# Kernel optimization log

Measured on AMD Instinct MI355X. Metric: run time of the kernel, lower is better.

The kernel has to match this reference:

```python
import jax, jax.numpy as jnp
import numpy as np
from jax.scipy.special import logsumexp

B, T, D = 16, 512, 768
S, H, O = 4, 48, 48
EMISS_W = 0.5  # args.emiss_nn_weight


def setup_inputs() -> dict:
    key = jax.random.key(0)
    ks = jax.random.split(key, 6)
    emb = jax.random.normal(ks[0], (B, T, D), jnp.float32)
    # obs must be valid per-source distributions over n_obs (log is taken)
    obs = jax.nn.softmax(2.0 * jax.random.normal(ks[1], (B, T, S, O), jnp.float32), axis=-1)
    # default prior init: priors = 0.001, priors[0] = 1, param = log(priors)
    p = jnp.full((H,), 0.001, jnp.float32).at[0].set(1.0)
    state_priors = jnp.log(p)
    unnorm_trans = jax.random.normal(ks[2], (H, H), jnp.float32)
    unnorm_emiss = jnp.zeros((S, H, O), jnp.float32)
    # xavier_uniform with relu gain for the per-source emission Linears
    bound = np.sqrt(2.0) * np.sqrt(6.0 / (D + H * O))
    W_emiss = jax.random.uniform(ks[3], (S, H * O, D), jnp.float32, -bound, bound)
    b_emiss = jnp.zeros((S, H * O), jnp.float32)
    seq_lengths = jax.random.randint(ks[4], (B,), T // 2, T + 1).astype(jnp.int32)
    seq_lengths = seq_lengths.at[0].set(T)  # max length == T
    return dict(emb=emb, obs=obs, state_priors=state_priors, unnorm_trans=unnorm_trans,
                unnorm_emiss=unnorm_emiss, W_emiss=W_emiss, b_emiss=b_emiss,
                seq_lengths=seq_lengths)


def _lognorm(x):
    return x - logsumexp(x, axis=-1, keepdims=True)


def reference(emb, obs, state_priors, unnorm_trans, unnorm_emiss, W_emiss, b_emiss, seq_lengths):
    lp = jax.nn.log_softmax(state_priors)                 # [H]
    log_trans = jax.nn.log_softmax(unnorm_trans, axis=-1)  # [H,H] (constant over b,t)
    emiss = jax.nn.softmax(unnorm_emiss, axis=-1)          # [S,H,O]

    # neural emissions: per-source Linear(d_emb -> H*O), softmax over O
    logits = jnp.einsum('btd,sod->btso', emb, W_emiss) + b_emiss  # [B,T,S,H*O]
    nn_emiss = jax.nn.softmax(logits.reshape(B, T, S, H, O), axis=-1)
    # (nn_trans is computed by NeuralModule in the original but discarded)

    log_emiss = jnp.log((1.0 - EMISS_W) * emiss[None, None] + EMISS_W * nn_emiss)  # [B,T,S,H,O]
    # log_matmul over obs axis, then sum over sources -> [B,T,H]
    lep = logsumexp(log_emiss + jnp.log(obs)[:, :, :, None, :], axis=-1).sum(axis=2)

    # forward recursion (normalized each step)
    a0 = _lognorm(lp + lep[:, 0])                          # [B,H]

    def fstep(a_prev, lep_t):
        a = _lognorm(lep_t + logsumexp(a_prev[:, :, None] + log_trans[None], axis=1))
        return a, a

    _, alphas = jax.lax.scan(fstep, a0, jnp.swapaxes(lep[:, 1:], 0, 1))
    log_alpha = jnp.concatenate([a0[:, None], jnp.swapaxes(alphas, 0, 1)], axis=1)  # [B,T,H]

    # backward recursion: beta[t] = logsumexp_j(trans[i,j] + lep[t,j] + beta[t+1,j])
    bT = jnp.zeros((B, H), lep.dtype)

    def bstep(b_next, lep_t):
        b = logsumexp(log_trans[None] + (lep_t + b_next)[:, None, :], axis=2)
        return b, b

    _, betas = jax.lax.scan(bstep, bT, jnp.swapaxes(lep[:, :T - 1], 0, 1), reverse=True)
    log_beta = jnp.concatenate([jnp.swapaxes(betas, 0, 1), bT[:, None]], axis=1)  # [B,T,H]
    # per-example roll by (length - T) along time, as in the original
    log_beta = jax.vmap(lambda b, s: jnp.roll(b, s, axis=0))(log_beta, seq_lengths - T)

    log_gamma = _lognorm(log_alpha + log_beta)             # [B,T,H]

    # xi_t = trans + alpha[t-1] (outer-sum) (lep[t] + beta[t]),  t = 1..T-1
    xi = (log_trans[None, None]
          + log_alpha[:, :-1, :, None]
          + (lep[:, 1:] + log_beta[:, 1:])[:, :, None, :])  # [B,T-1,H,H]
    xi = xi - logsumexp(xi, axis=(-2, -1), keepdims=True)

    log_prior = jnp.mean(jnp.sum(jnp.exp(log_gamma[:, 0]) * lp, axis=-1))

    tran_terms = jnp.sum(jnp.exp(xi) * log_trans[None, None], axis=(-2, -1))  # [B,T-1]
    mask_tr = (jnp.arange(T - 1)[None] < (seq_lengths - 1)[:, None]).astype(lep.dtype)
    log_tran = jnp.mean(jnp.sum(tran_terms * mask_tr, axis=1))

    emis_terms = jnp.sum(jnp.exp(log_gamma) * lep, axis=-1)  # [B,T]
    mask_em = (jnp.arange(T)[None] < seq_lengths[:, None]).astype(lep.dtype)
    log_emis = jnp.mean(jnp.sum(emis_terms * mask_em, axis=1))

    return log_prior + log_tran + log_emis
```

## Files before the change

### kernel.cpp

```cpp
#include <hip/hip_runtime.h>
#include <math.h>

namespace {

constexpr int Bn = 16, Tn = 512, Dn = 768, Sn = 4, Hn = 48, On = 48;
constexpr int Mn = Bn * Tn;
constexpr int Gn = Sn * Hn;
constexpr int Nn = Gn * On;
constexpr float EMISS_W = 0.5f;

constexpr size_t OFF_LP   = 0;
constexpr size_t OFF_LT   = 64;
constexpr size_t OFF_PT   = OFF_LT + Hn*Hn;
constexpr size_t OFF_EM   = OFF_PT + Hn*Hn;
constexpr size_t OFF_LEPP = OFF_EM + (size_t)Sn*Hn*On;
constexpr size_t OFF_LA   = OFF_LEPP + (size_t)Mn*Gn;
constexpr size_t OFF_LB   = OFF_LA + (size_t)Mn*Hn;
constexpr size_t OFF_RED  = OFF_LB + (size_t)Mn*Hn;
constexpr size_t FLOATS_END = OFF_RED + (size_t)Mn;

typedef __attribute__((ext_vector_type(8))) short short8;
typedef __attribute__((ext_vector_type(4))) float f32x4;

__device__ inline float waveSum(float v){
#pragma unroll
  for (int o = 32; o; o >>= 1) v += __shfl_xor(v, o);
  return v;
}

__device__ inline unsigned short f2bf(float f){
  unsigned int u = __float_as_uint(f);
  u += 0x7FFFu + ((u >> 16) & 1u);
  return (unsigned short)(u >> 16);
}

__device__ inline void gload_lds16(const void* g, void* l){
  __builtin_amdgcn_global_load_lds(
      (const __attribute__((address_space(1))) void*)g,
      (__attribute__((address_space(3))) void*)l, 16, 0, 0);
}

__global__ void convprep_kernel(const float* __restrict__ srcA, unsigned short* __restrict__ dstA,
                                int n4a,
                                const float* __restrict__ srcB, unsigned short* __restrict__ dstB,
                                int n4b,
                                const float* __restrict__ sp, const float* __restrict__ ut,
                                const float* __restrict__ ue, float* __restrict__ ws,
                                int nconv){
  const int tid = threadIdx.x;
  if ((int)blockIdx.x == nconv){
    float m = -INFINITY;
    for (int h = 0; h < Hn; ++h) m = fmaxf(m, sp[h]);
    float s = 0.f;
    for (int h = 0; h < Hn; ++h) s += __expf(sp[h] - m);
    float lse = m + __logf(s);
    if (tid < Hn) ws[OFF_LP + tid] = sp[tid] - lse;
    if (tid < Hn){
      const float* row = ut + tid * Hn;
      float mm = -INFINITY;
      for (int j = 0; j < Hn; ++j) mm = fmaxf(mm, row[j]);
      float ss = 0.f;
      for (int j = 0; j < Hn; ++j) ss += __expf(row[j] - mm);
      float l = mm + __logf(ss);
      for (int j = 0; j < Hn; ++j){
        float v = row[j] - l;
        ws[OFF_LT + tid*Hn + j] = v;
        ws[OFF_PT + tid*Hn + j] = __expf(v);
      }
    }
    for (int r = tid; r < Sn*Hn; r += blockDim.x){
      const float* row = ue + (size_t)r * On;
      float mm = -INFINITY;
      for (int o = 0; o < On; ++o) mm = fmaxf(mm, row[o]);
      float ss = 0.f;
      for (int o = 0; o < On; ++o) ss += __expf(row[o] - mm);
      float inv = 1.f/ss;
      for (int o = 0; o < On; ++o) ws[OFF_EM + (size_t)r*On + o] = __expf(row[o]-mm)*inv;
    }
    return;
  }
  int i = blockIdx.x * blockDim.x + tid;
  const float* s2; unsigned short* d; int k;
  if (i < n4a){ s2 = srcA; d = dstA; k = i; }
  else { k = i - n4a; if (k >= n4b) return; s2 = srcB; d = dstB; }
  float4 v = ((const float4*)s2)[k];
  ushort4 r;
  r.x = f2bf(v.x); r.y = f2bf(v.y); r.z = f2bf(v.z); r.w = f2bf(v.w);
  ((ushort4*)d)[k] = r;
}

constexpr int BM = 128, BN = 192, BK = 64;
constexpr int NKT = Dn / BK;

#define GEMM_BAR()  asm volatile("s_barrier" ::: "memory")
#define GEMM_LGKM() asm volatile("s_waitcnt lgkmcnt(0)" ::: "memory")

__global__ __launch_bounds__(256, 2) void gemm_lep_kernel(
    const unsigned short* __restrict__ embB, const unsigned short* __restrict__ WB,
    const float* __restrict__ bm, const float* __restrict__ obs,
    float* __restrict__ ws){
  __shared__ __align__(16) char smem[81920];
  const int tid = threadIdx.x, lane = tid & 63, w = tid >> 6;
  const int bid = blockIdx.y * (Mn/BM) + blockIdx.x;
  const int xcd = bid & 7, j_loc = bid >> 3;
  const int xm = xcd & 3, xn = xcd >> 2;
  const int mloc = j_loc & 15, nloc = j_loc >> 4;
  const int m0 = (xm*16 + mloc) * BM;
  const int by = xn*24 + nloc;
  const int N0 = by * BN;
  const int wm = w & 1, wn = w >> 1;
  const int lm = lane & 15, q = lane >> 4;
  const int key = lm & 7;
  const int srow = lane >> 3, spc = lane & 7;
  const int aoff0 = (q ^ key) << 4;
  const int aoff1 = ((4 + q) ^ key) << 4;

  f32x4 acc[4][6];
#pragma unroll
  for (int i = 0; i < 4; ++i)
#pragma unroll
    for (int j = 0; j < 6; ++j) acc[i][j] = (f32x4){0.f,0.f,0.f,0.f};

  auto stageA = [&](int kt, int i){
    const int idx = w*4 + i;
    const int row = idx*8 + srow;
    const int lc  = spc ^ (row & 7);
    gload_lds16(embB + (size_t)(m0+row)*Dn + kt*BK + lc*8,
                smem + (kt & 1)*16384 + idx*1024);
  };
  auto stageB = [&](int kt, int i){
    const int idx = w*6 + i;
    const int row = idx*8 + srow;
    const int lc  = spc ^ (row & 7);
    gload_lds16(WB + (size_t)(N0+row)*Dn + kt*BK + lc*8,
                smem + 32768 + (kt & 1)*24576 + idx*1024);
  };

#pragma unroll
  for (int i = 0; i < 4; ++i) stageA(0, i);
#pragma unroll
  for (int i = 0; i < 6; ++i) stageB(0, i);
  asm volatile("s_waitcnt vmcnt(0)" ::: "memory");
  GEMM_BAR();

  for (int kt = 0; kt < NKT; ++kt){
    const char* Ab = smem + (kt & 1)*16384;
    const char* Bb = smem + 32768 + (kt & 1)*24576;
    const int pf = kt + 1;
    const bool dopf = pf < NKT;
    short8 af[4], bf[3];

#pragma unroll
    for (int j = 0; j < 3; ++j)
      bf[j] = *(const short8*)(Bb + (wn*96 + j*16 + lm)*128 + aoff0);
#pragma unroll
    for (int i = 0; i < 4; ++i)
      af[i] = *(const short8*)(Ab + (wm*64 + i*16 + lm)*128 + aoff0);
    if (dopf){ stageA(pf,0); stageA(pf,1); stageA(pf,2); stageA(pf,3);
               stageB(pf,0); stageB(pf,1); }
    GEMM_BAR();
    GEMM_LGKM();
    __builtin_amdgcn_s_setprio(1);
#pragma unroll
    for (int i = 0; i < 4; ++i)
#pragma unroll
      for (int j = 0; j < 3; ++j)
        acc[i][j] = __builtin_amdgcn_mfma_f32_16x16x32_bf16(af[i], bf[j], acc[i][j], 0, 0, 0);
    __builtin_amdgcn_s_setprio(0);
    GEMM_BAR();

#pragma unroll
    for (int j = 0; j < 3; ++j)
      bf[j] = *(const short8*)(Bb + (wn*96 + (3+j)*16 + lm)*128 + aoff0);
    if (dopf){ stageB(pf,2); stageB(pf,3); }
    GEMM_BAR();
    GEMM_LGKM();
    __builtin_amdgcn_s_setprio(1);
#pragma unroll
    for (int i = 0; i < 4; ++i)
#pragma unroll
      for (int j = 0; j < 3; ++j)
        acc[i][3+j] = __builtin_amdgcn_mfma_f32_16x16x32_bf16(af[i], bf[j], acc[i][3+j], 0, 0, 0);
    __builtin_amdgcn_s_setprio(0);
    GEMM_BAR();

#pragma unroll
    for (int j = 0; j < 3; ++j)
      bf[j] = *(const short8*)(Bb + (wn*96 + j*16 + lm)*128 + aoff1);
#pragma unroll
    for (int i = 0; i < 4; ++i)
      af[i] = *(const short8*)(Ab + (wm*64 + i*16 + lm)*128 + aoff1);
    if (dopf){ stageB(pf,4); stageB(pf,5); }
    GEMM_BAR();
    GEMM_LGKM();
    __builtin_amdgcn_s_setprio(1);
#pragma unroll
    for (int i = 0; i < 4; ++i)
#pragma unroll
      for (int j = 0; j < 3; ++j)
        acc[i][j] = __builtin_amdgcn_mfma_f32_16x16x32_bf16(af[i], bf[j], acc[i][j], 0, 0, 0);
    __builtin_amdgcn_s_setprio(0);
    GEMM_BAR();

#pragma unroll
    for (int j = 0; j < 3; ++j)
      bf[j] = *(const short8*)(Bb + (wn*96 + (3+j)*16 + lm)*128 + aoff1);
    GEMM_BAR();
    GEMM_LGKM();
    __builtin_amdgcn_s_setprio(1);
#pragma unroll
    for (int i = 0; i < 4; ++i)
#pragma unroll
      for (int j = 0; j < 3; ++j)
        acc[i][3+j] = __builtin_amdgcn_mfma_f32_16x16x32_bf16(af[i], bf[j], acc[i][3+j], 0, 0, 0);
    __builtin_amdgcn_s_setprio(0);
    asm volatile("s_waitcnt vmcnt(0)" ::: "memory");
    GEMM_BAR();
  }

  float* Cp  = (float*)smem;
  float* ext = (float*)(smem + 49408);
  if (tid < 192){
    ext[tid]       = bm[N0 + tid];
    ext[192 + tid] = ws[OFF_EM + N0 + tid];
  }
#pragma unroll
  for (int h = 0; h < 2; ++h){
    if (h) __syncthreads();
    if (wm == h){
#pragma unroll
      for (int i = 0; i < 4; ++i)
#pragma unroll
        for (int j = 0; j < 6; ++j){
          const int col = wn*96 + j*16 + lm;
#pragma unroll
          for (int r = 0; r < 4; ++r){
            const int rowl = i*16 + q*4 + r;
            Cp[rowl*193 + col] = acc[i][j][r];
          }
        }
    }
    __syncthreads();
    {
      const int rowl = tid >> 2, grp = tid & 3;
      const int m = m0 + h*64 + rowl;
      const int g = by*4 + grp;
      const int s2 = g / Hn;
      const float* crow = Cp + rowl*193 + grp*48;
      const float* ob   = obs + ((size_t)m*Sn + s2)*On;
      const float* bi   = ext + grp*48;
      const float* em   = ext + 192 + grp*48;
      float Z = 0.f, pd = 0.f, eo = 0.f;
#pragma unroll
      for (int o = 0; o < On; ++o){
        float e = __expf(crow[o] + bi[o]);
        float obv = ob[o];
        Z += e;
        pd = fmaf(e, obv, pd);
        eo = fmaf(em[o], obv, eo);
      }
      ws[OFF_LEPP + (size_t)m*Gn + g] = __logf((1.f-EMISS_W)*eo + EMISS_W*(pd/Z));
    }
  }
}

constexpr int FBW = 24;
constexpr int FBL = 16;

__global__ __launch_bounds__(64) void fb_kernel(float* __restrict__ ws){
  __shared__ __align__(16) float ldsE[(FBW+FBL)*48];
  __shared__ __align__(16) float ring[2][64];
  const int lane = threadIdx.x;
  const int c    = blockIdx.x;
  const int b    = blockIdx.y;
  const bool fwd = blockIdx.z == 0;
  const bool act = lane < Hn;
  const int t0 = c*FBL, te = t0 + FBL - 1;

  float pt[Hn];
#pragma unroll
  for (int i = 0; i < Hn; ++i)
    pt[i] = act ? (fwd ? ws[OFF_PT + i*Hn + lane] : ws[OFF_PT + lane*Hn + i]) : 0.f;

  int row_lo, nrows, sA, sZ;
  bool exact;
  if (fwd){
    sA = t0 - FBW;
    exact = (sA < 1);
    row_lo = exact ? 0 : sA;
    if (exact) sA = 1;
    sZ = te;
    nrows = te - row_lo + 1;
  } else {
    int th = te + 1 + FBW;
    exact = (th > Tn - 2);
    sA = exact ? Tn - 2 : th - 1;
    sZ = t0;
    row_lo = t0;
    nrows = sA - t0 + 1;
  }

  {
    const float* src = ws + OFF_LEPP + ((size_t)b*Tn + row_lo)*Gn;
    int n4 = nrows * (Hn/4);
    for (int i = lane; i < n4; i += 64){
      int r = i / (Hn/4), h4 = i - r*(Hn/4);
      const float* p = src + (size_t)r*Gn + h4*4;
      float4 a = *(const float4*)(p);
      float4 b2 = *(const float4*)(p + Hn);
      float4 c2 = *(const float4*)(p + 2*Hn);
      float4 d2 = *(const float4*)(p + 3*Hn);
      float4 e;
      e.x = __expf(a.x + b2.x + c2.x + d2.x);
      e.y = __expf(a.y + b2.y + c2.y + d2.y);
      e.z = __expf(a.z + b2.z + c2.z + d2.z);
      e.w = __expf(a.w + b2.w + c2.w + d2.w);
      ((float4*)ldsE)[i] = e;
    }
  }
  __syncthreads();

  if (fwd){
    const size_t laF = OFF_LA + (size_t)b * Tn * Hn;
    float v;
    if (exact){
      v = act ? __expf(ws[OFF_LP + lane]) * ldsE[lane] : 0.f;
      if (c == 0 && act) ws[laF + lane] = v;
    } else {
      v = act ? 1.f : 0.f;
    }
    if (act) ring[0][lane] = v;
    __syncthreads();
    int cur = 0;
    for (int t = sA; t <= sZ; ++t){
      float S = waveSum(v);
      const float* rp = ring[cur];
      float s0=0.f,s1=0.f,s2=0.f,s3=0.f;
#pragma unroll
      for (int i = 0; i < Hn; i += 4){
        float4 a = *(const float4*)(rp + i);
        s0 = fmaf(a.x, pt[i+0], s0); s1 = fmaf(a.y, pt[i+1], s1);
        s2 = fmaf(a.z, pt[i+2], s2); s3 = fmaf(a.w, pt[i+3], s3);
      }
      float sd = (s0+s1)+(s2+s3);
      float e = act ? ldsE[(t - row_lo)*Hn + lane] : 0.f;
      float vn = act ? e * sd * (1.f/S) : 0.f;
      cur ^= 1;
      if (act) ring[cur][lane] = vn;
      __syncthreads();
      if (act && t >= t0) ws[laF + (size_t)t*Hn + lane] = vn;
      v = vn;
    }
  } else {
    const size_t lbF = OFF_LB + (size_t)b * Tn * Hn;
    float v = act ? 1.f : 0.f;
    if (exact && c == (Tn/FBL - 1) && act) ws[lbF + (size_t)(Tn-1)*Hn + lane] = 1.f;
    int cur = 0;
    for (int t = sA; t >= sZ; --t){
      float e = act ? ldsE[(t - row_lo)*Hn + lane] : 0.f;
      float wv = e * v;
      if (act) ring[cur][lane] = wv;
      float S = waveSum(wv);
      __syncthreads();
      const float* rp = ring[cur];
      float s0=0.f,s1=0.f,s2=0.f,s3=0.f;
#pragma unroll
      for (int j = 0; j < Hn; j += 4){
        float4 a = *(const float4*)(rp + j);
        s0 = fmaf(a.x, pt[j+0], s0); s1 = fmaf(a.y, pt[j+1], s1);
        s2 = fmaf(a.z, pt[j+2], s2); s3 = fmaf(a.w, pt[j+3], s3);
      }
      float vn = act ? ((s0+s1)+(s2+s3)) * (1.f/S) : 0.f;
      cur ^= 1;
      if (act && t <= te) ws[lbF + (size_t)t*Hn + lane] = vn;
      v = vn;
    }
  }
}

__global__ __launch_bounds__(256) void gamma_xi_kernel(
    const float* __restrict__ ws_c, float* __restrict__ ws,
    const int* __restrict__ seq_len){
  __shared__ float y_s[Hn], lap_s[Hn];
  __shared__ float red[8];
  const int tid = threadIdx.x;
  const int bid = blockIdx.x;
  const int b = bid >> 9, t = bid & (Tn-1);
  const int len = seq_len[b];
  int tb = t + (Tn - len); if (tb >= Tn) tb -= Tn;
  const size_t bt = (size_t)b*Tn + t;
  float lep = 0.f;
  if (tid < Hn){
    const float* lpp = ws_c + OFF_LEPP + bt*Gn + tid;
    lep = lpp[0] + lpp[Hn] + lpp[2*Hn] + lpp[3*Hn];
    float lb  = ws_c[OFF_LB + ((size_t)b*Tn + tb)*Hn + tid];
    y_s[tid] = __expf(lep) * lb;
    if (t >= 1) lap_s[tid] = ws_c[OFF_LA + (bt-1)*Hn + tid];
  }
  float emis_term = 0.f, prior_term = 0.f;
  if (tid < 64){
    int h = (tid < Hn) ? tid : 0;
    float la  = ws_c[OFF_LA + bt*Hn + h];
    float lb  = ws_c[OFF_LB + ((size_t)b*Tn + tb)*Hn + h];
    float lp  = ws_c[OFF_LP + h];
    float wgt = (tid < Hn) ? la*lb : 0.f;
    float Z = waveSum(wgt);
    float inv = 1.f / Z;
    emis_term  = waveSum(wgt * lep) * inv;
    prior_term = waveSum(wgt * lp) * inv;
  }
  __syncthreads();
  float tran_term = 0.f;
  if (t >= 1){
    float se = 0.f, st = 0.f;
#pragma unroll
    for (int k=0;k<9;++k){
      int e = tid + k*256;
      int i = e / Hn, j = e - i*Hn;
      float e2 = ws_c[OFF_PT + e] * lap_s[i] * y_s[j];
      se += e2;
      st = fmaf(e2, ws_c[OFF_LT + e], st);
    }
    se = waveSum(se);
    st = waveSum(st);
    const int wid = tid >> 6;
    if ((tid & 63) == 0){ red[wid] = se; red[4+wid] = st; }
    __syncthreads();
    if (tid == 0){
      float SE = red[0]+red[1]+red[2]+red[3];
      float ST = red[4]+red[5]+red[6]+red[7];
      tran_term = ST / SE;
    }
  }
  if (tid == 0){
    float tot = 0.f;
    if (t < len)            tot += emis_term;
    if (t == 0)             tot += prior_term;
    if (t >= 1 && t < len)  tot += tran_term;
    ws[OFF_RED + bid] = tot;
  }
}

__global__ __launch_bounds__(256) void sum_kernel(const float* __restrict__ ws,
                                                  float* __restrict__ out){
  __shared__ float red[4];
  const int tid = threadIdx.x;
  float s = 0.f;
  for (int i = tid; i < Mn; i += 256) s += ws[OFF_RED + i];
  s = waveSum(s);
  if ((tid & 63) == 0) red[tid >> 6] = s;
  __syncthreads();
  if (tid == 0) out[0] = (red[0]+red[1]+red[2]+red[3]) * (1.f / Bn);
}

}

extern "C" void kernel_launch(void* const* d_in, const int* in_sizes, int n_in,
                              void* d_out, int out_size, void* d_ws, size_t ws_size,
                              hipStream_t stream){
  const float* emb = (const float*)d_in[0];
  const float* obs = (const float*)d_in[1];
  const float* sp  = (const float*)d_in[2];
  const float* ut  = (const float*)d_in[3];
  const float* ue  = (const float*)d_in[4];
  const float* Wm  = (const float*)d_in[5];
  const float* bm  = (const float*)d_in[6];
  const int*   sl  = (const int*)d_in[7];
  float* ws  = (float*)d_ws;
  float* out = (float*)d_out;
  (void)in_sizes; (void)n_in; (void)ws_size; (void)out_size;

  unsigned short* embB = (unsigned short*)(ws + FLOATS_END);
  unsigned short* WB   = embB + (size_t)Mn * Dn;

  const int n4a = Mn*Dn/4, n4b = Nn*Dn/4;
  const int nconv = (n4a + n4b + 255)/256;
  convprep_kernel<<<nconv + 1, 256, 0, stream>>>(emb, embB, n4a, Wm, WB, n4b,
                                                 sp, ut, ue, ws, nconv);
  gemm_lep_kernel<<<dim3(Mn/BM, Nn/BN), 256, 0, stream>>>(embB, WB, bm, obs, ws);
  fb_kernel<<<dim3(Tn/FBL, Bn, 2), 64, 0, stream>>>(ws);
  gamma_xi_kernel<<<Bn*Tn, 256, 0, stream>>>(ws, ws, sl);
  sum_kernel<<<1, 256, 0, stream>>>(ws, out);
}
```

Baseline: 294.5 us.

## Collapse GEMM k-loop phases into one barrier with all fragments loaded upfront

The bf16 MFMA main loop drops its four-phase structure, which interleaved LDS fragment loads, partial prefetch and priority-boosted MFMA groups between many s_barriers. Each iteration now waits on vmcnt and one barrier, loads all A/B fragments for the whole BK tile into registers, issues the full next-tile prefetch, then runs all 48 MFMAs back to back. The goal is to cut barrier and synchronisation overhead. In exchange it holds roughly twice as many fragment registers live, which may hurt occupancy at launch_bounds(256,2), and it loses the fine-grained overlap of loads with MFMA inside each wave.

Result: faster. 288.7 us (-2.0%).

```diff
diff --git a/kernel.cpp b/kernel.cpp
--- a/kernel.cpp
+++ b/kernel.cpp
@@ -92,9 +92,6 @@
 constexpr int BM = 128, BN = 192, BK = 64;
 constexpr int NKT = Dn / BK;
 
-#define GEMM_BAR()  asm volatile("s_barrier" ::: "memory")
-#define GEMM_LGKM() asm volatile("s_waitcnt lgkmcnt(0)" ::: "memory")
-
 __global__ __launch_bounds__(256, 2) void gemm_lep_kernel(
     const unsigned short* __restrict__ embB, const unsigned short* __restrict__ WB,
     const float* __restrict__ bm, const float* __restrict__ obs,
@@ -140,84 +137,67 @@
   for (int i = 0; i < 4; ++i) stageA(0, i);
 #pragma unroll
   for (int i = 0; i < 6; ++i) stageB(0, i);
-  asm volatile("s_waitcnt vmcnt(0)" ::: "memory");
-  GEMM_BAR();
 
   for (int kt = 0; kt < NKT; ++kt){
     const char* Ab = smem + (kt & 1)*16384;
     const char* Bb = smem + 32768 + (kt & 1)*24576;
+
+    asm volatile("s_waitcnt vmcnt(0)" ::: "memory");
+    asm volatile("s_barrier" ::: "memory");
+
+    short8 a0[4], a1[4], b0[3], b1[3], b2[3], b3[3];
+#pragma unroll
+    for (int j = 0; j < 3; ++j)
+      b0[j] = *(const short8*)(Bb + (wn*96 + j*16 + lm)*128 + aoff0);
+#pragma unroll
+    for (int i = 0; i < 4; ++i)
+      a0[i] = *(const short8*)(Ab + (wm*64 + i*16 + lm)*128 + aoff0);
+#pragma unroll
+    for (int j = 0; j < 3; ++j)
+      b1[j] = *(const short8*)(Bb + (wn*96 + (3+j)*16 + lm)*128 + aoff0);
+#pragma unroll
+    for (int i = 0; i < 4; ++i)
+      a1[i] = *(const short8*)(Ab + (wm*64 + i*16 + lm)*128 + aoff1);
+#pragma unroll
+    for (int j = 0; j < 3; ++j)
+      b2[j] = *(const short8*)(Bb + (wn*96 + j*16 + lm)*128 + aoff1);
+#pragma unroll
+    for (int j = 0; j < 3; ++j)
+      b3[j] = *(const short8*)(Bb + (wn*96 + (3+j)*16 + lm)*128 + aoff1);
+
     const int pf = kt + 1;
-    const bool dopf = pf < NKT;
-    short8 af[4], bf[3];
-
-#pragma unroll
-    for (int j = 0; j < 3; ++j)
-      bf[j] = *(const short8*)(Bb + (wn*96 + j*16 + lm)*128 + aoff0);
-#pragma unroll
-    for (int i = 0; i < 4; ++i)
-      af[i] = *(const short8*)(Ab + (wm*64 + i*16 + lm)*128 + aoff0);
-    if (dopf){ stageA(pf,0); stageA(pf,1); stageA(pf,2); stageA(pf,3);
-               stageB(pf,0); stageB(pf,1); }
-    GEMM_BAR();
-    GEMM_LGKM();
+    if (pf < NKT){
+#pragma unroll
+      for (int i = 0; i < 4; ++i) stageA(pf, i);
+#pragma unroll
+      for (int i = 0; i < 6; ++i) stageB(pf, i);
+    }
+
     __builtin_amdgcn_s_setprio(1);
 #pragma unroll
     for (int i = 0; i < 4; ++i)
 #pragma unroll
       for (int j = 0; j < 3; ++j)
-        acc[i][j] = __builtin_amdgcn_mfma_f32_16x16x32_bf16(af[i], bf[j], acc[i][j], 0, 0, 0);
+        acc[i][j] = __builtin_amdgcn_mfma_f32_16x16x32_bf16(a0[i], b0[j], acc[i][j], 0, 0, 0);
+#pragma unroll
+    for (int i = 0; i < 4; ++i)
+#pragma unroll
+      for (int j = 0; j < 3; ++j)
+        acc[i][3+j] = __builtin_amdgcn_mfma_f32_16x16x32_bf16(a0[i], b1[j], acc[i][3+j], 0, 0, 0);
+#pragma unroll
+    for (int i = 0; i < 4; ++i)
+#pragma unroll
+      for (int j = 0; j < 3; ++j)
+        acc[i][j] = __builtin_amdgcn_mfma_f32_16x16x32_bf16(a1[i], b2[j], acc[i][j], 0, 0, 0);
+#pragma unroll
+    for (int i = 0; i < 4; ++i)
+#pragma unroll
+      for (int j = 0; j < 3; ++j)
+        acc[i][3+j] = __builtin_amdgcn_mfma_f32_16x16x32_bf16(a1[i], b3[j], acc[i][3+j], 0, 0, 0);
     __builtin_amdgcn_s_setprio(0);
-    GEMM_BAR();
-
-#pragma unroll
-    for (int j = 0; j < 3; ++j)
-      bf[j] = *(const short8*)(Bb + (wn*96 + (3+j)*16 + lm)*128 + aoff0);
-    if (dopf){ stageB(pf,2); stageB(pf,3); }
-    GEMM_BAR();
-    GEMM_LGKM();
-    __builtin_amdgcn_s_setprio(1);
-#pragma unroll
-    for (int i = 0; i < 4; ++i)
-#pragma unroll
-      for (int j = 0; j < 3; ++j)
-        acc[i][3+j] = __builtin_amdgcn_mfma_f32_16x16x32_bf16(af[i], bf[j], acc[i][3+j], 0, 0, 0);
-    __builtin_amdgcn_s_setprio(0);
-    GEMM_BAR();
-
-#pragma unroll
-    for (int j = 0; j < 3; ++j)
-      bf[j] = *(const short8*)(Bb + (wn*96 + j*16 + lm)*128 + aoff1);
-#pragma unroll
-    for (int i = 0; i < 4; ++i)
-      af[i] = *(const short8*)(Ab + (wm*64 + i*16 + lm)*128 + aoff1);
-    if (dopf){ stageB(pf,4); stageB(pf,5); }
-    GEMM_BAR();
-    GEMM_LGKM();
-    __builtin_amdgcn_s_setprio(1);
-#pragma unroll
-    for (int i = 0; i < 4; ++i)
-#pragma unroll
-      for (int j = 0; j < 3; ++j)
-        acc[i][j] = __builtin_amdgcn_mfma_f32_16x16x32_bf16(af[i], bf[j], acc[i][j], 0, 0, 0);
-    __builtin_amdgcn_s_setprio(0);
-    GEMM_BAR();
-
-#pragma unroll
-    for (int j = 0; j < 3; ++j)
-      bf[j] = *(const short8*)(Bb + (wn*96 + (3+j)*16 + lm)*128 + aoff1);
-    GEMM_BAR();
-    GEMM_LGKM();
-    __builtin_amdgcn_s_setprio(1);
-#pragma unroll
-    for (int i = 0; i < 4; ++i)
-#pragma unroll
-      for (int j = 0; j < 3; ++j)
-        acc[i][3+j] = __builtin_amdgcn_mfma_f32_16x16x32_bf16(af[i], bf[j], acc[i][3+j], 0, 0, 0);
-    __builtin_amdgcn_s_setprio(0);
-    asm volatile("s_waitcnt vmcnt(0)" ::: "memory");
-    GEMM_BAR();
-  }
-
+  }
+
+  __syncthreads();
   float* Cp  = (float*)smem;
   float* ext = (float*)(smem + 49408);
   if (tid < 192){
```
